# Performance work log

Hardware: AMD Instinct MI355X
Metric: run time of the kernel (lower is better)

Reference implementation:

```python
import jax, jax.numpy as jnp
import numpy as np

HID = 1024
IN = 17


def _lstm_cell(x, h, c, W_ih, W_hh, b_ih, b_hh):
    # PyTorch LSTMCell: gates = x@W_ih.T + b_ih + h@W_hh.T + b_hh
    g = x @ W_ih.T + h @ W_hh.T + (b_ih + b_hh)
    i, f, gg, o = jnp.split(g, 4, axis=-1)
    i = jax.nn.sigmoid(i)
    f = jax.nn.sigmoid(f)
    gg = jnp.tanh(gg)
    o = jax.nn.sigmoid(o)
    c_new = f * c + i * gg
    h_new = o * jnp.tanh(c_new)
    return h_new, c_new


def setup_inputs() -> dict:
    key = jax.random.key(0)
    ks = jax.random.split(key, 12)
    B, T = 4096, 19
    s_ih1 = 1.0 / np.sqrt(IN)
    s_h = 1.0 / np.sqrt(HID)
    return {
        "x": jax.random.normal(ks[0], (B, T, IN), jnp.float32),
        "W_ih1": jax.random.normal(ks[1], (4 * HID, IN), jnp.float32) * s_ih1,
        "W_hh1": jax.random.normal(ks[2], (4 * HID, HID), jnp.float32) * s_h,
        "b_ih1": jax.random.normal(ks[3], (4 * HID,), jnp.float32) * s_h,
        "b_hh1": jax.random.normal(ks[4], (4 * HID,), jnp.float32) * s_h,
        "W_ih2": jax.random.normal(ks[5], (4 * HID, HID), jnp.float32) * s_h,
        "W_hh2": jax.random.normal(ks[6], (4 * HID, HID), jnp.float32) * s_h,
        "b_ih2": jax.random.normal(ks[7], (4 * HID,), jnp.float32) * s_h,
        "b_hh2": jax.random.normal(ks[8], (4 * HID,), jnp.float32) * s_h,
        "W_lin": jax.random.normal(ks[9], (IN, HID), jnp.float32) * s_h,
        "b_lin": jax.random.normal(ks[10], (IN,), jnp.float32) * s_h,
    }


def reference(x, W_ih1, W_hh1, b_ih1, b_hh1, W_ih2, W_hh2, b_ih2, b_hh2, W_lin, b_lin):
    B = x.shape[0]
    h1 = jnp.zeros((B, HID), x.dtype)
    c1 = jnp.zeros((B, HID), x.dtype)
    h2 = jnp.zeros((B, HID), x.dtype)
    c2 = jnp.zeros((B, HID), x.dtype)

    xt = jnp.transpose(x, (1, 0, 2))  # (T, B, IN)

    def step(carry, x_t):
        h1, c1, h2, c2 = carry
        h1, c1 = _lstm_cell(x_t, h1, c1, W_ih1, W_hh1, b_ih1, b_hh1)
        h2, c2 = _lstm_cell(h1, h2, c2, W_ih2, W_hh2, b_ih2, b_hh2)
        out = h2 @ W_lin.T + b_lin
        return (h1, c1, h2, c2), out

    _, outs = jax.lax.scan(step, (h1, c1, h2, c2), xt)  # (T, B, IN)
    return jnp.transpose(outs, (1, 0, 2))  # (B, T, IN)
```

## Files before the change

### kernel.cpp

```cpp
#include <hip/hip_runtime.h>

#define HID     1024
#define TSTEPS  19
#define INDIM   17
#define XSTRIDE (TSTEPS * INDIM)

typedef unsigned short u16;
typedef unsigned int   u32;
typedef __attribute__((ext_vector_type(8))) _Float16 f16x8;
typedef __attribute__((ext_vector_type(4))) float f32x4;

__device__ __forceinline__ u16 f2h(float f) {
    union { _Float16 h; u16 u; } v; v.h = (_Float16)f; return v.u;
}
__device__ __forceinline__ float h2f(u16 x) {
    union { _Float16 h; u16 u; } v; v.u = x; return (float)v.h;
}
__device__ __forceinline__ float sigm(float x) {
    x = fminf(fmaxf(x, -30.f), 30.f);
    return 1.f / (1.f + __expf(-x));
}
__device__ __forceinline__ float tanhr(float x) {
    x = fminf(fmaxf(x, -15.f), 15.f);
    float e = __expf(-2.f * x);
    return (1.f - e) / (1.f + e);
}

__device__ __forceinline__ void gload_lds16(const u16* g, u16* l) {
    __builtin_amdgcn_global_load_lds(
        (const __attribute__((address_space(1))) u32*)g,
        (__attribute__((address_space(3))) u32*)l, 16, 0, 0);
}

#define NW4 1048576
__global__ __launch_bounds__(256) void split4_kernel(
    const float* __restrict__ a, u16* __restrict__ ah,
    const float* __restrict__ b, u16* __restrict__ bh,
    const float* __restrict__ c, u16* __restrict__ ch,
    const float* __restrict__ d, u16* __restrict__ dh, int nd4)
{
    int i = blockIdx.x * blockDim.x + threadIdx.x;
    const float* src; u16* dst; int off;
    if (i < NW4)               { src = a; dst = ah; off = i; }
    else if (i < 2 * NW4)      { src = b; dst = bh; off = i - NW4; }
    else if (i < 3 * NW4)      { src = c; dst = ch; off = i - 2 * NW4; }
    else if (i < 3 * NW4 + nd4){ src = d; dst = dh; off = i - 3 * NW4; }
    else return;
    float4 v = ((const float4*)src)[off];
    ushort4 h;
    h.x = f2h(v.x); h.y = f2h(v.y); h.z = f2h(v.z); h.w = f2h(v.w);
    ((ushort4*)dst)[off] = h;
}

__global__ __launch_bounds__(256) void pack_x_kernel(
    const float* __restrict__ x, u16* __restrict__ xpack)
{
    const int i = blockIdx.x * blockDim.x + threadIdx.x;
    if (i >= TSTEPS * 4096) return;
    const int t = i >> 12, b = i & 4095;
    const float* src = x + (size_t)b * XSTRIDE + (size_t)t * INDIM;
    u16 row[64];
#pragma unroll
    for (int k = 0; k < INDIM; ++k) {
        const float v = src[k];
        const u16 hi = f2h(v);
        row[k] = hi;
        row[INDIM + k] = f2h(v - h2f(hi));
        row[2 * INDIM + k] = hi;
    }
#pragma unroll
    for (int k = 3 * INDIM; k < 64; ++k) row[k] = 0;
    uint4* dst = (uint4*)(xpack + (size_t)i * 64);
#pragma unroll
    for (int q = 0; q < 8; ++q) dst[q] = ((const uint4*)row)[q];
}

__global__ __launch_bounds__(256) void pack_wx_kernel(
    const float* __restrict__ W, u16* __restrict__ wxpack)
{
    const int n = blockIdx.x * blockDim.x + threadIdx.x;
    if (n >= 4 * HID) return;
    const float* src = W + (size_t)n * INDIM;
    u16 row[64];
#pragma unroll
    for (int k = 0; k < INDIM; ++k) {
        const float v = src[k];
        const u16 hi = f2h(v);
        row[k] = hi;
        row[INDIM + k] = hi;
        row[2 * INDIM + k] = f2h(v - h2f(hi));
    }
#pragma unroll
    for (int k = 3 * INDIM; k < 64; ++k) row[k] = 0;
    uint4* dst = (uint4*)(wxpack + (size_t)n * 64);
#pragma unroll
    for (int q = 0; q < 8; ++q) dst[q] = ((const uint4*)row)[q];
}

__device__ __forceinline__ void gate_body(
    u16* lA, u16* lB, int rb, int u0,
    const u16* __restrict__ a0, const u16* __restrict__ w0,
    const u16* __restrict__ a1, const u16* __restrict__ w1,
    const u16* __restrict__ xp, const u16* __restrict__ wxp,
    const float* __restrict__ bi, const float* __restrict__ bh,
    float* __restrict__ cbuf, u16* __restrict__ outh,
    int first, int nsrc)
{
    const int tid  = threadIdx.x;
    const int wave = tid >> 6;
    const int lane = tid & 63;
    const int col  = lane & 15;
    const int quad = lane >> 4;

    const int lr = lane >> 3;
    const int ck = (lane & 7) ^ lr;

    f32x4 acc[4][8];
    const f32x4 fzero = {0.f, 0.f, 0.f, 0.f};
#pragma unroll
    for (int i = 0; i < 4; ++i)
#pragma unroll
        for (int j = 0; j < 8; ++j) acc[i][j] = fzero;

    const int nst = nsrc << 4;
    const int ntot = nst + (xp ? 1 : 0);
    for (int s = 0; s < ntot; ++s) {
        const bool isx = (s >= nst);
        const u16* Asrc = isx ? xp  : ((s < 16) ? a0 : a1);
        const u16* Wsrc = isx ? wxp : ((s < 16) ? w0 : w1);
        const int k0 = isx ? 0 : (s & 15) * 64;
        const int st = isx ? 64 : HID;

        __syncthreads();
#pragma unroll
        for (int i = 0; i < 8; ++i) {
            const int rbase = wave * 64 + i * 8;
            const int r = rbase + lr;
            const u16* gp = Asrc + (size_t)(rb + r) * st + k0 + ck * 8;
            gload_lds16(gp, lA + rbase * 64);
        }
#pragma unroll
        for (int i = 0; i < 4; ++i) {
            const int vbase = wave * 32 + i * 8;
            const int v = vbase + lr;
            const int n = ((v >> 5) << 10) + u0 + (v & 31);
            const u16* gp = Wsrc + (size_t)n * st + k0 + ck * 8;
            gload_lds16(gp, lB + vbase * 64);
        }
        __syncthreads();

#pragma unroll
        for (int ks = 0; ks < 2; ++ks) {
            const int p = ((ks << 2) + quad) ^ (col & 7);
            f16x8 av[4], bv[8];
#pragma unroll
            for (int rf = 0; rf < 4; ++rf)
                av[rf] = *(const f16x8*)(lA + (wave * 64 + rf * 16 + col) * 64 + p * 8);
#pragma unroll
            for (int cf = 0; cf < 8; ++cf)
                bv[cf] = *(const f16x8*)(lB + (cf * 16 + col) * 64 + p * 8);
#pragma unroll
            for (int rf = 0; rf < 4; ++rf)
#pragma unroll
                for (int cf = 0; cf < 8; ++cf)
                    acc[rf][cf] = __builtin_amdgcn_mfma_f32_16x16x32_f16(
                        av[rf], bv[cf], acc[rf][cf], 0, 0, 0);
        }
    }

#pragma unroll
    for (int s2 = 0; s2 < 2; ++s2) {
        const int u = u0 + s2 * 16 + col;
        const float bI = bi[u]           + bh[u];
        const float bF = bi[HID + u]     + bh[HID + u];
        const float bG = bi[2 * HID + u] + bh[2 * HID + u];
        const float bO = bi[3 * HID + u] + bh[3 * HID + u];
#pragma unroll
        for (int rf = 0; rf < 4; ++rf) {
#pragma unroll
            for (int rr = 0; rr < 4; ++rr) {
                const int brow = rb + wave * 64 + rf * 16 + quad * 4 + rr;
                const size_t idx = (size_t)brow * HID + u;
                const float iv = sigm(acc[rf][0 + s2][rr] + bI);
                const float fv = sigm(acc[rf][2 + s2][rr] + bF);
                const float gv = tanhr(acc[rf][4 + s2][rr] + bG);
                const float ov = sigm(acc[rf][6 + s2][rr] + bO);
                const float cold = first ? 0.f : cbuf[idx];
                const float cn = fv * cold + iv * gv;
                const float hn = ov * tanhr(cn);
                cbuf[idx] = cn;
                outh[idx] = f2h(hn);
            }
        }
    }
}

__device__ __forceinline__ void out_body8(int oid,
    const u16* __restrict__ h2h,
    const u16* __restrict__ Wlin, const float* __restrict__ blin,
    float* __restrict__ out, int t)
{
    const int tid = threadIdx.x;
    const int wave = tid >> 6, lane = tid & 63;
    const int r = lane >> 5, q = lane & 31;
    const int b = oid * 8 + wave * 2 + r;
    const u16* hh = h2h + (size_t)b * HID;
    float acc[INDIM];
#pragma unroll
    for (int j = 0; j < INDIM; ++j) acc[j] = 0.f;
#pragma unroll 2
    for (int it = 0; it < 8; ++it) {
        const int u = q * 32 + it * 4;
        const ushort4 a = *(const ushort4*)(hh + u);
        const float h0 = h2f(a.x), h1 = h2f(a.y), h2 = h2f(a.z), h3 = h2f(a.w);
#pragma unroll
        for (int j = 0; j < INDIM; ++j) {
            const ushort4 w = *(const ushort4*)(Wlin + j * HID + u);
            acc[j] += h0 * h2f(w.x) + h1 * h2f(w.y)
                    + h2 * h2f(w.z) + h3 * h2f(w.w);
        }
    }
#pragma unroll
    for (int j = 0; j < INDIM; ++j) {
        float v = acc[j];
        v += __shfl_xor(v, 1);
        v += __shfl_xor(v, 2);
        v += __shfl_xor(v, 4);
        v += __shfl_xor(v, 8);
        v += __shfl_xor(v, 16);
        acc[j] = v;
    }
    const size_t ob = (size_t)b * XSTRIDE + (size_t)t * INDIM;
    float mine = acc[0];
#pragma unroll
    for (int j = 1; j < INDIM; ++j) if (q == j) mine = acc[j];
    if (q < INDIM) out[ob + q] = mine + blin[q];
}

__global__ __launch_bounds__(256, 2) void step_kernel(
    int doA, int doB,
    const u16* __restrict__ Aa0, const u16* __restrict__ Aw0,
    const u16* __restrict__ Aa1, const u16* __restrict__ Aw1,
    const float* __restrict__ Abi, const float* __restrict__ Abh,
    float* __restrict__ Acbuf, u16* __restrict__ Aouth, int Afirst, int Ansrc,
    const u16* __restrict__ Ba0, const u16* __restrict__ Bw0,
    const u16* __restrict__ Bxp, const u16* __restrict__ Bwxp,
    const float* __restrict__ Bbi, const float* __restrict__ Bbh,
    float* __restrict__ Bcbuf, u16* __restrict__ Bouth, int Bfirst, int Bnsrc,
    const u16* __restrict__ Oh2, const u16* __restrict__ Wlin,
    const float* __restrict__ blin, float* __restrict__ outp, int Ot)
{
    __shared__ u16 lA[256 * 64];
    __shared__ u16 lB[128 * 64];
    const int bid = blockIdx.x;
    const int rb  = (bid >> 5) * 256;
    const int u0  = ((bid & 7) * 4 + ((bid >> 3) & 3)) * 32;
    const auto runA = [&]() {
        gate_body(lA, lB, rb, u0, Aa0, Aw0, Aa1, Aw1, nullptr, nullptr,
                  Abi, Abh, Acbuf, Aouth, Afirst, Ansrc);
    };
    const auto runB = [&]() {
        gate_body(lA, lB, rb, u0, Ba0, Bw0, nullptr, nullptr, Bxp, Bwxp,
                  Bbi, Bbh, Bcbuf, Bouth, Bfirst, Bnsrc);
    };
    if (bid & 1) { if (doB) runB(); if (doA) runA(); }
    else         { if (doA) runA(); if (doB) runB(); }
    if (Ot >= 0)
        out_body8(bid, Oh2, Wlin, blin, outp, Ot);
}

extern "C" void kernel_launch(void* const* d_in, const int* in_sizes, int n_in,
                              void* d_out, int out_size, void* d_ws, size_t ws_size,
                              hipStream_t stream)
{
    const float* x     = (const float*)d_in[0];
    const float* W_ih1 = (const float*)d_in[1];
    const float* W_hh1 = (const float*)d_in[2];
    const float* b_ih1 = (const float*)d_in[3];
    const float* b_hh1 = (const float*)d_in[4];
    const float* W_ih2 = (const float*)d_in[5];
    const float* W_hh2 = (const float*)d_in[6];
    const float* b_ih2 = (const float*)d_in[7];
    const float* b_hh2 = (const float*)d_in[8];
    const float* W_lin = (const float*)d_in[9];
    const float* b_lin = (const float*)d_in[10];
    float* out = (float*)d_out;
    char* ws = (char*)d_ws;
    const size_t MB = (size_t)1 << 20;

    float* c1 = (float*)(ws);
    float* c2 = (float*)(ws + 16 * MB);
    u16* h1[4] = { (u16*)(ws + 32 * MB), (u16*)(ws + 40 * MB),
                   (u16*)(ws + 48 * MB), (u16*)(ws + 56 * MB) };
    u16* h2[4] = { (u16*)(ws + 64 * MB), (u16*)(ws + 72 * MB),
                   (u16*)(ws + 80 * MB), (u16*)(ws + 88 * MB) };
    u16* w1h    = (u16*)(ws + 96 * MB);
    u16* w2ih   = (u16*)(ws + 104 * MB);
    u16* w2hh   = (u16*)(ws + 112 * MB);
    u16* xpack  = (u16*)(ws + 120 * MB);
    u16* wxpack = (u16*)(ws + 130 * MB);
    u16* wlin16 = (u16*)(ws + 131 * MB);

    const int nWlin4 = INDIM * HID / 4;
    const int nTot = 3 * NW4 + nWlin4;
    split4_kernel<<<(nTot + 255) / 256, 256, 0, stream>>>(
        W_hh1, w1h, W_ih2, w2ih, W_hh2, w2hh, W_lin, wlin16, nWlin4);
    pack_x_kernel<<<(TSTEPS * 4096 + 255) / 256, 256, 0, stream>>>(x, xpack);
    pack_wx_kernel<<<(4 * HID + 255) / 256, 256, 0, stream>>>(W_ih1, wxpack);

    for (int s = 0; s <= TSTEPS + 1; ++s) {
        const int ta = s - 1, tb = s, to = s - 2;
        const int doA = (s >= 1 && s <= TSTEPS) ? 1 : 0;
        const int doB = (s <= TSTEPS - 1) ? 1 : 0;
        step_kernel<<<512, 256, 0, stream>>>(
            doA, doB,
            h1[ta & 3], w2ih, h2[(ta + 3) & 3], w2hh, b_ih2, b_hh2,
            c2, h2[ta & 3], (ta == 0) ? 1 : 0, (ta == 0) ? 1 : 2,
            h1[(tb + 3) & 3], w1h,
            xpack + (size_t)(tb < 0 ? 0 : tb) * 4096 * 64, wxpack,
            b_ih1, b_hh1,
            c1, h1[tb & 3], (tb == 0) ? 1 : 0, (tb == 0) ? 0 : 1,
            h2[to & 3], wlin16, b_lin, out, to);
    }
    (void)in_sizes; (void)n_in; (void)out_size; (void)ws_size;
}
```

Before: 2.437 ms.

## Software-pipeline LDS loads with triple-buffered weights and register-held activations

```diff
diff --git a/kernel.cpp b/kernel.cpp
--- a/kernel.cpp
+++ b/kernel.cpp
@@ -115,6 +115,9 @@
     const int lr = lane >> 3;
     const int ck = (lane & 7) ^ lr;
 
+    const int nst = nsrc << 4;
+    const int ntot = nst + (xp ? 1 : 0);
+
     f32x4 acc[4][8];
     const f32x4 fzero = {0.f, 0.f, 0.f, 0.f};
 #pragma unroll
@@ -122,50 +125,75 @@
 #pragma unroll
         for (int j = 0; j < 8; ++j) acc[i][j] = fzero;
 
-    const int nst = nsrc << 4;
-    const int ntot = nst + (xp ? 1 : 0);
-    for (int s = 0; s < ntot; ++s) {
+    auto issueA = [&](int s) {
         const bool isx = (s >= nst);
-        const u16* Asrc = isx ? xp  : ((s < 16) ? a0 : a1);
+        const u16* Asrc = isx ? xp : ((s < 16) ? a0 : a1);
+        const int k0 = isx ? 0 : (s & 15) * 64;
+        const int st = isx ? 64 : HID;
+#pragma unroll
+        for (int i = 0; i < 8; ++i) {
+            const int rbase = wave * 64 + i * 8;
+            const u16* gp = Asrc + (size_t)(rb + rbase + lr) * st + k0 + ck * 8;
+            gload_lds16(gp, lA + rbase * 64);
+        }
+    };
+    auto issueB = [&](int s) {
+        const bool isx = (s >= nst);
         const u16* Wsrc = isx ? wxp : ((s < 16) ? w0 : w1);
         const int k0 = isx ? 0 : (s & 15) * 64;
         const int st = isx ? 64 : HID;
-
-        __syncthreads();
-#pragma unroll
-        for (int i = 0; i < 8; ++i) {
-            const int rbase = wave * 64 + i * 8;
-            const int r = rbase + lr;
-            const u16* gp = Asrc + (size_t)(rb + r) * st + k0 + ck * 8;
-            gload_lds16(gp, lA + rbase * 64);
-        }
+        u16* dst = lB + (s % 3) * (128 * 64);
 #pragma unroll
         for (int i = 0; i < 4; ++i) {
             const int vbase = wave * 32 + i * 8;
             const int v = vbase + lr;
             const int n = ((v >> 5) << 10) + u0 + (v & 31);
             const u16* gp = Wsrc + (size_t)n * st + k0 + ck * 8;
-            gload_lds16(gp, lB + vbase * 64);
-        }
-        __syncthreads();
-
+            gload_lds16(gp, dst + vbase * 64);
+        }
+    };
+
+    __builtin_amdgcn_s_barrier();
+    issueA(0);
+    issueB(0);
+    if (ntot > 1) issueB(1);
+
+    for (int s = 0; s < ntot; ++s) {
+        if (s < ntot - 1) asm volatile("s_waitcnt vmcnt(4)" ::: "memory");
+        else              asm volatile("s_waitcnt vmcnt(0)" ::: "memory");
+        __builtin_amdgcn_s_barrier();
+
+        f16x8 av[2][4];
+#pragma unroll
+        for (int ks = 0; ks < 2; ++ks) {
+            const int pa = ((ks << 2) + quad) ^ (col & 7);
+#pragma unroll
+            for (int rf = 0; rf < 4; ++rf)
+                av[ks][rf] = *(const f16x8*)(lA + (wave * 64 + rf * 16 + col) * 64 + pa * 8);
+        }
+        asm volatile("s_waitcnt lgkmcnt(0)" ::: "memory");
+        __builtin_amdgcn_sched_barrier(0);
+
+        if (s + 1 < ntot) issueA(s + 1);
+        if (s + 2 < ntot) issueB(s + 2);
+
+        const u16* lBr = lB + (s % 3) * (128 * 64);
+        __builtin_amdgcn_s_setprio(1);
 #pragma unroll
         for (int ks = 0; ks < 2; ++ks) {
             const int p = ((ks << 2) + quad) ^ (col & 7);
-            f16x8 av[4], bv[8];
-#pragma unroll
-            for (int rf = 0; rf < 4; ++rf)
-                av[rf] = *(const f16x8*)(lA + (wave * 64 + rf * 16 + col) * 64 + p * 8);
+            f16x8 bv[8];
 #pragma unroll
             for (int cf = 0; cf < 8; ++cf)
-                bv[cf] = *(const f16x8*)(lB + (cf * 16 + col) * 64 + p * 8);
+                bv[cf] = *(const f16x8*)(lBr + (cf * 16 + col) * 64 + p * 8);
 #pragma unroll
             for (int rf = 0; rf < 4; ++rf)
 #pragma unroll
                 for (int cf = 0; cf < 8; ++cf)
                     acc[rf][cf] = __builtin_amdgcn_mfma_f32_16x16x32_f16(
-                        av[rf], bv[cf], acc[rf][cf], 0, 0, 0);
-        }
+                        av[ks][rf], bv[cf], acc[rf][cf], 0, 0, 0);
+        }
+        __builtin_amdgcn_s_setprio(0);
     }
 
 #pragma unroll
@@ -251,7 +279,7 @@
     const float* __restrict__ blin, float* __restrict__ outp, int Ot)
 {
     __shared__ u16 lA[256 * 64];
-    __shared__ u16 lB[128 * 64];
+    __shared__ u16 lB[3 * 128 * 64];
     const int bid = blockIdx.x;
     const int rb  = (bid >> 5) * 256;
     const int u0  = ((bid & 7) * 4 + ((bid >> 3) & 3)) * 32;
```

Result: slower. 5.197 ms (+113.3%).

## Load A operand fragments directly from global memory, dropping LDS staging

Applied to the files above, without the earlier changes.

```diff
diff --git a/kernel.cpp b/kernel.cpp
--- a/kernel.cpp
+++ b/kernel.cpp
@@ -98,7 +98,7 @@
 }
 
 __device__ __forceinline__ void gate_body(
-    u16* lA, u16* lB, int rb, int u0,
+    u16* lB, int rb, int u0,
     const u16* __restrict__ a0, const u16* __restrict__ w0,
     const u16* __restrict__ a1, const u16* __restrict__ w1,
     const u16* __restrict__ xp, const u16* __restrict__ wxp,
@@ -133,13 +133,6 @@
 
         __syncthreads();
 #pragma unroll
-        for (int i = 0; i < 8; ++i) {
-            const int rbase = wave * 64 + i * 8;
-            const int r = rbase + lr;
-            const u16* gp = Asrc + (size_t)(rb + r) * st + k0 + ck * 8;
-            gload_lds16(gp, lA + rbase * 64);
-        }
-#pragma unroll
         for (int i = 0; i < 4; ++i) {
             const int vbase = wave * 32 + i * 8;
             const int v = vbase + lr;
@@ -151,11 +144,13 @@
 
 #pragma unroll
         for (int ks = 0; ks < 2; ++ks) {
+            const u16* abase = Asrc + (size_t)(rb + wave * 64 + col) * st
+                             + k0 + (ks * 4 + quad) * 8;
+            f16x8 av[4], bv[8];
+#pragma unroll
+            for (int rf = 0; rf < 4; ++rf)
+                av[rf] = *(const f16x8*)(abase + (size_t)rf * 16 * st);
             const int p = ((ks << 2) + quad) ^ (col & 7);
-            f16x8 av[4], bv[8];
-#pragma unroll
-            for (int rf = 0; rf < 4; ++rf)
-                av[rf] = *(const f16x8*)(lA + (wave * 64 + rf * 16 + col) * 64 + p * 8);
 #pragma unroll
             for (int cf = 0; cf < 8; ++cf)
                 bv[cf] = *(const f16x8*)(lB + (cf * 16 + col) * 64 + p * 8);
@@ -168,29 +163,41 @@
         }
     }
 
-#pragma unroll
-    for (int s2 = 0; s2 < 2; ++s2) {
-        const int u = u0 + s2 * 16 + col;
-        const float bI = bi[u]           + bh[u];
-        const float bF = bi[HID + u]     + bh[HID + u];
-        const float bG = bi[2 * HID + u] + bh[2 * HID + u];
-        const float bO = bi[3 * HID + u] + bh[3 * HID + u];
-#pragma unroll
-        for (int rf = 0; rf < 4; ++rf) {
-#pragma unroll
-            for (int rr = 0; rr < 4; ++rr) {
-                const int brow = rb + wave * 64 + rf * 16 + quad * 4 + rr;
-                const size_t idx = (size_t)brow * HID + u;
-                const float iv = sigm(acc[rf][0 + s2][rr] + bI);
-                const float fv = sigm(acc[rf][2 + s2][rr] + bF);
-                const float gv = tanhr(acc[rf][4 + s2][rr] + bG);
-                const float ov = sigm(acc[rf][6 + s2][rr] + bO);
-                const float cold = first ? 0.f : cbuf[idx];
-                const float cn = fv * cold + iv * gv;
-                const float hn = ov * tanhr(cn);
-                cbuf[idx] = cn;
-                outh[idx] = f2h(hn);
-            }
+    const int u_a = u0 + col;
+    const int u_b = u0 + 16 + col;
+    const float bIa = bi[u_a]           + bh[u_a];
+    const float bFa = bi[HID + u_a]     + bh[HID + u_a];
+    const float bGa = bi[2 * HID + u_a] + bh[2 * HID + u_a];
+    const float bOa = bi[3 * HID + u_a] + bh[3 * HID + u_a];
+    const float bIb = bi[u_b]           + bh[u_b];
+    const float bFb = bi[HID + u_b]     + bh[HID + u_b];
+    const float bGb = bi[2 * HID + u_b] + bh[2 * HID + u_b];
+    const float bOb = bi[3 * HID + u_b] + bh[3 * HID + u_b];
+#pragma unroll
+    for (int rf = 0; rf < 4; ++rf) {
+#pragma unroll
+        for (int rr = 0; rr < 4; ++rr) {
+            const int brow = rb + wave * 64 + rf * 16 + quad * 4 + rr;
+            const size_t idx0 = (size_t)brow * HID + u_a;
+            const size_t idx1 = idx0 + 16;
+            const float iva = sigm(acc[rf][0][rr] + bIa);
+            const float fva = sigm(acc[rf][2][rr] + bFa);
+            const float gva = tanhr(acc[rf][4][rr] + bGa);
+            const float ova = sigm(acc[rf][6][rr] + bOa);
+            const float ivb = sigm(acc[rf][1][rr] + bIb);
+            const float fvb = sigm(acc[rf][3][rr] + bFb);
+            const float gvb = tanhr(acc[rf][5][rr] + bGb);
+            const float ovb = sigm(acc[rf][7][rr] + bOb);
+            const float colda = first ? 0.f : cbuf[idx0];
+            const float coldb = first ? 0.f : cbuf[idx1];
+            const float cna = fva * colda + iva * gva;
+            const float cnb = fvb * coldb + ivb * gvb;
+            const float hna = ova * tanhr(cna);
+            const float hnb = ovb * tanhr(cnb);
+            cbuf[idx0] = cna;
+            cbuf[idx1] = cnb;
+            outh[idx0] = f2h(hna);
+            outh[idx1] = f2h(hnb);
         }
     }
 }
@@ -250,17 +257,16 @@
     const u16* __restrict__ Oh2, const u16* __restrict__ Wlin,
     const float* __restrict__ blin, float* __restrict__ outp, int Ot)
 {
-    __shared__ u16 lA[256 * 64];
     __shared__ u16 lB[128 * 64];
     const int bid = blockIdx.x;
     const int rb  = (bid >> 5) * 256;
     const int u0  = ((bid & 7) * 4 + ((bid >> 3) & 3)) * 32;
     const auto runA = [&]() {
-        gate_body(lA, lB, rb, u0, Aa0, Aw0, Aa1, Aw1, nullptr, nullptr,
+        gate_body(lB, rb, u0, Aa0, Aw0, Aa1, Aw1, nullptr, nullptr,
                   Abi, Abh, Acbuf, Aouth, Afirst, Ansrc);
     };
     const auto runB = [&]() {
-        gate_body(lA, lB, rb, u0, Ba0, Bw0, nullptr, nullptr, Bxp, Bwxp,
+        gate_body(lB, rb, u0, Ba0, Bw0, nullptr, nullptr, Bxp, Bwxp,
                   Bbi, Bbh, Bcbuf, Bouth, Bfirst, Bnsrc);
     };
     if (bid & 1) { if (doB) runB(); if (doA) runA(); }
```

New measurement: 3.020 ms. 23.9% more time.
